# Performance work log

Measured on AMD Instinct MI355X. Metric: run time of the kernel, lower is better.

## Reference

```python
import jax, jax.numpy as jnp
import numpy as np

B, S, D, H = 8, 2048, 1024, 128  # batch, seq (== CONTEXT_WINDOW), embed dim, headspace


def setup_inputs() -> dict:
    key = jax.random.key(0)
    ks = jax.random.split(key, 7)
    scale = 1.0 / np.sqrt(D)
    return {
        "x": jax.random.normal(ks[0], (B, S, D), dtype=jnp.float32),
        "Wq": jax.random.normal(ks[1], (D, H), dtype=jnp.float32) * scale,
        "bq": jax.random.normal(ks[2], (H,), dtype=jnp.float32) * 0.01,
        "Wk": jax.random.normal(ks[3], (D, H), dtype=jnp.float32) * scale,
        "bk": jax.random.normal(ks[4], (H,), dtype=jnp.float32) * 0.01,
        "Wv": jax.random.normal(ks[5], (D, H), dtype=jnp.float32) * scale,
        "bv": jax.random.normal(ks[6], (H,), dtype=jnp.float32) * 0.01,
    }


def reference(x, Wq, bq, Wk, bk, Wv, bv):
    # x: [B, S, D]
    embedlen = x.shape[-1]
    q = x @ Wq + bq  # [B, S, H]
    k = x @ Wk + bk  # [B, S, H]
    v = x @ Wv + bv  # [B, S, H]
    # NOTE: original code MULTIPLIES by sqrt(embedlen) (embedlen = full embed dim) --
    # faithful reproduction of the source, not the standard 1/sqrt(head_dim).
    scale = jnp.sqrt(jnp.asarray(embedlen, dtype=x.dtype))
    scores = jnp.einsum("bsh,bth->bst", q, k) * scale  # [B, S, S]
    seqlen = x.shape[1]
    causal = jnp.tril(jnp.ones((seqlen, seqlen), dtype=bool))
    scores = jnp.where(causal, scores, -jnp.inf)
    attn = jax.nn.softmax(scores, axis=-1)
    return jnp.einsum("bst,bth->bsh", attn, v)  # [B, S, H]
```

## Files before the change

kernel.cpp:

```cpp
#include <hip/hip_runtime.h>
#include <math.h>

#define SEQ 2048
#define DIM 1024
#define HD  128
#define NB  8
#define M_TOT (NB * SEQ)

typedef __attribute__((ext_vector_type(8))) short   short8;
typedef __attribute__((ext_vector_type(4))) short   short4v;
typedef __attribute__((ext_vector_type(4))) float   floatx4;

__device__ __forceinline__ unsigned short f2bf(float f) {
    unsigned u = __builtin_bit_cast(unsigned, f);
    u += 0x7FFFu + ((u >> 16) & 1u);
    return (unsigned short)(u >> 16);
}
__device__ __forceinline__ float bf2f(unsigned short h) {
    unsigned u = ((unsigned)h) << 16;
    return __builtin_bit_cast(float, u);
}
__device__ __forceinline__ void async16(const void* g, void* l) {
    __builtin_amdgcn_global_load_lds(
        (const __attribute__((address_space(1))) unsigned int*)g,
        (__attribute__((address_space(3))) unsigned int*)l, 16, 0, 0);
}

#define MFMA16(a, b, c) __builtin_amdgcn_mfma_f32_16x16x32_bf16((a), (b), (c), 0, 0, 0)

__global__ __launch_bounds__(256) void wt_prep(
    const float* __restrict__ Wq, const float* __restrict__ Wk, const float* __restrict__ Wv,
    unsigned short* __restrict__ Wth, unsigned short* __restrict__ Wtl)
{
    int idx = blockIdx.x * 256 + threadIdx.x;
    int k   = idx & 1023;
    int n   = (idx >> 10) & 127;
    int mat = idx >> 17;
    const float* W = (mat == 0) ? Wq : (mat == 1) ? Wk : Wv;
    float v = W[k * HD + n];
    unsigned short hi = f2bf(v);
    Wth[idx] = hi;
    Wtl[idx] = f2bf(v - bf2f(hi));
}

__global__ __launch_bounds__(512, 4) void qkv_fused(
    const float* __restrict__ x,
    const unsigned short* __restrict__ Wth, const unsigned short* __restrict__ Wtl,
    const float* __restrict__ bq, const float* __restrict__ bk, const float* __restrict__ bv,
    unsigned short* __restrict__ Qh, unsigned short* __restrict__ Ql,
    unsigned short* __restrict__ Kh, unsigned short* __restrict__ Kl,
    unsigned short* __restrict__ Vt)
{
    __shared__ short lds[56 * 512];

    const int t    = threadIdx.x;
    const int lane = t & 63;
    const int w    = t >> 6;
    const int lrow = lane & 15;
    const int quad = lane >> 4;

    const int R0 = blockIdx.x * 64;
    const int z  = blockIdx.y;
    const int mh = w & 1;
    const int nh = w >> 1;

    auto stageB = [&](int k0, int qb) {
        #pragma unroll
        for (int i = 0; i < 3; ++i) {
            int f = i * 8 + w;
            if (f < 20) {
                int p   = (f >= 12);
                int ff  = p ? (f - 12) : f;
                int mat = ff >> 2, nfl = ff & 3;
                const unsigned short* src = (p ? Wtl : Wth) + (size_t)mat * (HD * DIM)
                    + (size_t)((z * 4 + nfl) * 16 + lrow) * DIM + k0 + quad * 8;
                async16(src, &lds[(qb * 28 + 8 + f) * 512 + lane * 8]);
            }
        }
    };

    const int arow = t >> 3;
    const int akk  = (t & 7) * 4;
    auto xload = [&](int k0) -> float4 {
        return *(const float4*)&x[(size_t)(R0 + arow) * DIM + k0 + akk];
    };
    auto stageA = [&](float4 xv, int qb) {
        float xf[4] = {xv.x, xv.y, xv.z, xv.w};
        short4v hv, lv;
        #pragma unroll
        for (int j = 0; j < 4; ++j) {
            unsigned short h = f2bf(xf[j]);
            hv[j] = (short)h;
            lv[j] = (short)f2bf(xf[j] - bf2f(h));
        }
        int mi = arow >> 4, lr = arow & 15, qd = akk >> 3, el = akk & 7;
        int base = (qb * 28 + mi * 2) * 512 + (qd * 16 + lr) * 8 + el;
        *(short4v*)&lds[base]       = hv;
        *(short4v*)&lds[base + 512] = lv;
    };

    floatx4 acc[2][3];
    const floatx4 zf = {0.f, 0.f, 0.f, 0.f};
    #pragma unroll
    for (int mi2 = 0; mi2 < 2; ++mi2)
        #pragma unroll
        for (int c = 0; c < 3; ++c) acc[mi2][c] = zf;

    auto compute = [&](int qb) {
        short8 a[2][2];
        #pragma unroll
        for (int mi2 = 0; mi2 < 2; ++mi2)
            #pragma unroll
            for (int p = 0; p < 2; ++p)
                a[mi2][p] = *(short8*)&lds[(qb * 28 + (mh * 2 + mi2) * 2 + p) * 512 + lane * 8];

        short8 bhq = *(short8*)&lds[(qb * 28 + 8 +  0 + nh) * 512 + lane * 8];
        short8 bhk = *(short8*)&lds[(qb * 28 + 8 +  4 + nh) * 512 + lane * 8];
        short8 bhv = *(short8*)&lds[(qb * 28 + 8 +  8 + nh) * 512 + lane * 8];
        short8 blq = *(short8*)&lds[(qb * 28 + 20 + 0 + nh) * 512 + lane * 8];
        short8 blk = *(short8*)&lds[(qb * 28 + 20 + 4 + nh) * 512 + lane * 8];

        #pragma unroll
        for (int mi2 = 0; mi2 < 2; ++mi2) {
            acc[mi2][0] = MFMA16(a[mi2][0], bhq, acc[mi2][0]);
            acc[mi2][1] = MFMA16(a[mi2][0], bhk, acc[mi2][1]);
            acc[mi2][2] = MFMA16(a[mi2][0], bhv, acc[mi2][2]);
            acc[mi2][0] = MFMA16(a[mi2][1], bhq, acc[mi2][0]);
            acc[mi2][1] = MFMA16(a[mi2][1], bhk, acc[mi2][1]);
            acc[mi2][0] = MFMA16(a[mi2][0], blq, acc[mi2][0]);
            acc[mi2][1] = MFMA16(a[mi2][0], blk, acc[mi2][1]);
        }
    };

    stageB(0, 0);
    stageA(xload(0), 0);
    float4 xn0 = xload(32);
    float4 xn1 = xload(64);

    for (int it = 0; it < 32; ++it) {
        __syncthreads();
        const int k0 = it * 32;
        const int q  = it & 1;

        if (it < 31) {
            stageB(k0 + 32, q ^ 1);
            stageA(xn0, q ^ 1);
            xn0 = xn1;
            int kx = (k0 + 96 <= DIM - 32) ? (k0 + 96) : (DIM - 32);
            xn1 = xload(kx);
        }

        compute(q);
    }

    const int col = (z * 4 + nh) * 16 + lrow;
    const float bqv = bq[col], bkv = bk[col], bvv = bv[col];
    #pragma unroll
    for (int mi2 = 0; mi2 < 2; ++mi2) {
        #pragma unroll
        for (int reg = 0; reg < 4; ++reg) {
            int gm = R0 + (mh * 2 + mi2) * 16 + quad * 4 + reg;
            float vq = (acc[mi2][0][reg] + bqv) * 32.0f;
            unsigned short h = f2bf(vq);
            Qh[(size_t)gm * HD + col] = h;
            Ql[(size_t)gm * HD + col] = f2bf(vq - bf2f(h));
            float vk = acc[mi2][1][reg] + bkv;
            h = f2bf(vk);
            Kh[(size_t)gm * HD + col] = h;
            Kl[(size_t)gm * HD + col] = f2bf(vk - bf2f(h));
            float vv = acc[mi2][2][reg] + bvv;
            int b = gm >> 11, s = gm & 2047;
            Vt[((size_t)b * HD + col) * SEQ + s] = f2bf(vv);
        }
    }
}

__global__ __launch_bounds__(256) void flash_attn(
    const unsigned short* __restrict__ Qh, const unsigned short* __restrict__ Ql,
    const unsigned short* __restrict__ Kh, const unsigned short* __restrict__ Kl,
    const unsigned short* __restrict__ Vt, float* __restrict__ out,
    float* __restrict__ Opart, float* __restrict__ ML, int split)
{
    __shared__ short lds[52 * 512];

    const int t    = threadIdx.x;
    const int lane = t & 63;
    const int w    = t >> 6;
    const int lrow = lane & 15;
    const int quad = lane >> 4;

    const int idx = blockIdx.x;
    const int b   = idx & 7;
    const int h   = split ? ((idx >> 3) & 1) : 0;
    const int s   = split ? (63 - (idx >> 4)) : (63 - (idx >> 3));
    const int T   = (s + 2) >> 1;
    const int Th  = (T + 1) >> 1;
    const int t0  = split ? (h ? Th : 0) : 0;
    const int t1  = split ? (h ? T : Th) : T;

    if (split && t0 >= t1) {
        float* op = Opart + (size_t)idx * 4096;
        for (int i = t; i < 4096; i += 256) op[i] = 0.0f;
        if (t < 32) { ML[(idx * 32 + t) * 2] = -1e30f; ML[(idx * 32 + t) * 2 + 1] = 0.0f; }
        return;
    }

    const int mh = w & 1;
    const int kh = w >> 1;
    const int R  = s * 32 + mh * 16;

    const size_t kbase = (size_t)b * SEQ * HD;
    const size_t vbase = (size_t)b * HD * SEQ;

    short8 qf[4][2];
    #pragma unroll
    for (int kc = 0; kc < 4; ++kc) {
        size_t off = kbase + (size_t)(R + lrow) * HD + kc * 32 + quad * 8;
        qf[kc][0] = *(const short8*)(Qh + off);
        qf[kc][1] = *(const short8*)(Ql + off);
    }

    const floatx4 zf = {0.f, 0.f, 0.f, 0.f};
    floatx4 accO[8];
    #pragma unroll
    for (int i = 0; i < 8; ++i) accO[i] = zf;
    float m_[4] = {-1e30f, -1e30f, -1e30f, -1e30f};
    float l_[4] = {0.f, 0.f, 0.f, 0.f};

    for (int it = t0; it < t1; ++it) {
        const int j0 = it * 64;
        __syncthreads();
        #pragma unroll
        for (int i = 0; i < 12; ++i) {
            int id = w * 12 + i;
            const unsigned short* src;
            if (id < 32) {
                int nt = id >> 3, kc = (id >> 1) & 3, p = id & 1;
                src = (p ? Kl : Kh) + kbase
                    + (size_t)(j0 + nt * 16 + lrow) * HD + kc * 32 + quad * 8;
            } else {
                int v = id - 32, df = v >> 1, kc = v & 1;
                src = Vt + vbase + (size_t)(df * 16 + lrow) * SEQ
                    + j0 + kc * 32 + quad * 8;
            }
            async16(src, &lds[id * 512 + lane * 8]);
        }
        __syncthreads();

        floatx4 S[2] = {zf, zf};
        #pragma unroll
        for (int ntl = 0; ntl < 2; ++ntl) {
            int nt = kh * 2 + ntl;
            #pragma unroll
            for (int kc = 0; kc < 4; ++kc) {
                short8 khf = *(short8*)&lds[(nt * 8 + kc * 2 + 0) * 512 + lane * 8];
                short8 klf = *(short8*)&lds[(nt * 8 + kc * 2 + 1) * 512 + lane * 8];
                S[ntl] = MFMA16(qf[kc][0], khf, S[ntl]);
                S[ntl] = MFMA16(qf[kc][0], klf, S[ntl]);
                S[ntl] = MFMA16(qf[kc][1], khf, S[ntl]);
            }
        }
        if (j0 + kh * 32 + 31 > R) {
            #pragma unroll
            for (int ntl = 0; ntl < 2; ++ntl) {
                int key = j0 + (kh * 2 + ntl) * 16 + lrow;
                #pragma unroll
                for (int reg = 0; reg < 4; ++reg) {
                    if (key > R + quad * 4 + reg) S[ntl][reg] = -INFINITY;
                }
            }
        }
        float alpha[4];
        #pragma unroll
        for (int reg = 0; reg < 4; ++reg) {
            float mx = fmaxf(S[0][reg], S[1][reg]);
            #pragma unroll
            for (int hh = 1; hh < 16; hh <<= 1) mx = fmaxf(mx, __shfl_xor(mx, hh));
            float mnew = fmaxf(fmaxf(m_[reg], mx), -1e30f);
            alpha[reg] = __expf(m_[reg] - mnew);
            m_[reg] = mnew;
            float p0 = __expf(S[0][reg] - mnew);
            float p1 = __expf(S[1][reg] - mnew);
            S[0][reg] = p0; S[1][reg] = p1;
            float ls = p0 + p1;
            #pragma unroll
            for (int hh = 1; hh < 16; hh <<= 1) ls += __shfl_xor(ls, hh);
            l_[reg] = l_[reg] * alpha[reg] + ls;
        }
        #pragma unroll
        for (int i = 0; i < 8; ++i)
            #pragma unroll
            for (int reg = 0; reg < 4; ++reg) accO[i][reg] *= alpha[reg];

        #pragma unroll
        for (int ntl = 0; ntl < 2; ++ntl) {
            #pragma unroll
            for (int reg = 0; reg < 4; ++reg) {
                int kloc = ntl * 16 + lrow;
                int jj = kloc & 7, q2 = (kloc >> 3) & 3;
                int lane2 = (quad * 4 + reg) + (q2 << 4);
                lds[(48 + w) * 512 + lane2 * 8 + jj] = (short)f2bf(S[ntl][reg]);
            }
        }
        short8 pf = *(short8*)&lds[(48 + w) * 512 + lane * 8];
        #pragma unroll
        for (int df = 0; df < 8; ++df) {
            short8 vf = *(short8*)&lds[(32 + df * 2 + kh) * 512 + lane * 8];
            accO[df] = MFMA16(pf, vf, accO[df]);
        }
    }

    __syncthreads();
    float* fl   = (float*)lds;
    float* Obuf = fl;
    float* mlb  = fl + 4096;
    if (lrow == 0) {
        #pragma unroll
        for (int reg = 0; reg < 4; ++reg) {
            int row = quad * 4 + reg;
            mlb[((kh * 2 + mh) * 16 + row) * 2 + 0] = m_[reg];
            mlb[((kh * 2 + mh) * 16 + row) * 2 + 1] = l_[reg];
        }
    }
    __syncthreads();
    float myw[4], Mrow[4], Drow[4];
    #pragma unroll
    for (int reg = 0; reg < 4; ++reg) {
        int row = quad * 4 + reg;
        float mo  = mlb[(((1 - kh) * 2 + mh) * 16 + row) * 2 + 0];
        float lo_ = mlb[(((1 - kh) * 2 + mh) * 16 + row) * 2 + 1];
        float M = fmaxf(m_[reg], mo);
        float d = l_[reg] * __expf(m_[reg] - M) + lo_ * __expf(mo - M);
        Mrow[reg] = M; Drow[reg] = d;
        myw[reg] = split ? __expf(m_[reg] - M) : (__expf(m_[reg] - M) / d);
    }
    if (kh == 0) {
        #pragma unroll
        for (int df = 0; df < 8; ++df)
            #pragma unroll
            for (int reg = 0; reg < 4; ++reg)
                Obuf[(mh * 16 + quad * 4 + reg) * 128 + df * 16 + lrow] =
                    accO[df][reg] * myw[reg];
    }
    __syncthreads();
    if (kh == 1) {
        if (split) {
            float* op = Opart + (size_t)idx * 4096;
            #pragma unroll
            for (int df = 0; df < 8; ++df) {
                #pragma unroll
                for (int reg = 0; reg < 4; ++reg) {
                    int row = mh * 16 + quad * 4 + reg;
                    op[row * 128 + df * 16 + lrow] =
                        Obuf[row * 128 + df * 16 + lrow] + accO[df][reg] * myw[reg];
                }
            }
            if (lrow == 0) {
                #pragma unroll
                for (int reg = 0; reg < 4; ++reg) {
                    int row = mh * 16 + quad * 4 + reg;
                    ML[(idx * 32 + row) * 2 + 0] = Mrow[reg];
                    ML[(idx * 32 + row) * 2 + 1] = Drow[reg];
                }
            }
        } else {
            #pragma unroll
            for (int df = 0; df < 8; ++df) {
                #pragma unroll
                for (int reg = 0; reg < 4; ++reg) {
                    float v = Obuf[(mh * 16 + quad * 4 + reg) * 128 + df * 16 + lrow]
                            + accO[df][reg] * myw[reg];
                    size_t o = ((size_t)(b * SEQ + R + quad * 4 + reg)) * HD + df * 16 + lrow;
                    out[o] = v;
                }
            }
        }
    }
}

__global__ __launch_bounds__(256) void splitk_merge(
    const float* __restrict__ Opart, const float* __restrict__ ML,
    float* __restrict__ out)
{
    int tid = blockIdx.x * 256 + threadIdx.x;
    int row = tid >> 5, c4 = tid & 31;
    int b = row >> 11, r = row & 2047, s = r >> 5, rr = r & 31;
    int i0 = ((63 - s) << 4) + b;
    int i1 = i0 + 8;
    float m0 = ML[(i0 * 32 + rr) * 2], l0 = ML[(i0 * 32 + rr) * 2 + 1];
    float m1 = ML[(i1 * 32 + rr) * 2], l1 = ML[(i1 * 32 + rr) * 2 + 1];
    float M  = fmaxf(m0, m1);
    float w0 = __expf(m0 - M), w1 = __expf(m1 - M);
    float inv = 1.0f / (w0 * l0 + w1 * l1);
    float4 a  = *(const float4*)&Opart[((size_t)i0 * 32 + rr) * 128 + c4 * 4];
    float4 bb = *(const float4*)&Opart[((size_t)i1 * 32 + rr) * 128 + c4 * 4];
    float4 o;
    o.x = (w0 * a.x + w1 * bb.x) * inv;
    o.y = (w0 * a.y + w1 * bb.y) * inv;
    o.z = (w0 * a.z + w1 * bb.z) * inv;
    o.w = (w0 * a.w + w1 * bb.w) * inv;
    *(float4*)&out[(size_t)row * 128 + c4 * 4] = o;
}

extern "C" void kernel_launch(void* const* d_in, const int* in_sizes, int n_in,
                              void* d_out, int out_size, void* d_ws, size_t ws_size,
                              hipStream_t stream) {
    const float* x  = (const float*)d_in[0];
    const float* Wq = (const float*)d_in[1];
    const float* bq = (const float*)d_in[2];
    const float* Wk = (const float*)d_in[3];
    const float* bk = (const float*)d_in[4];
    const float* Wv = (const float*)d_in[5];
    const float* bv = (const float*)d_in[6];
    float* out = (float*)d_out;

    unsigned short* Qh  = (unsigned short*)d_ws;
    unsigned short* Ql  = Qh  + (size_t)M_TOT * HD;
    unsigned short* Kh  = Ql  + (size_t)M_TOT * HD;
    unsigned short* Kl  = Kh  + (size_t)M_TOT * HD;
    unsigned short* Vt  = Kl  + (size_t)M_TOT * HD;
    unsigned short* Wth = Vt  + (size_t)M_TOT * HD;
    unsigned short* Wtl = Wth + (size_t)3 * HD * DIM;
    float* Opart = (float*)(Wtl + (size_t)3 * HD * DIM);
    float* ML    = Opart + (size_t)1024 * 32 * 128;

    const size_t need = 22544384ULL + 16777216ULL + 262144ULL;
    const int split = (ws_size >= need) ? 1 : 0;

    wt_prep<<<(3 * HD * DIM) / 256, 256, 0, stream>>>(Wq, Wk, Wv, Wth, Wtl);
    qkv_fused<<<dim3(256, 2), 512, 0, stream>>>(x, Wth, Wtl, bq, bk, bv, Qh, Ql, Kh, Kl, Vt);
    flash_attn<<<split ? 1024 : 512, 256, 0, stream>>>(Qh, Ql, Kh, Kl, Vt, out, Opart, ML, split);
    if (split) splitk_merge<<<2048, 256, 0, stream>>>(Opart, ML, out);
}
```

Baseline: 218.5 us.

## Load V fragments directly from global into registers instead of staging in LDS

V tiles are no longer staged into shared memory with async copies. Each wave now loads its V MFMA fragments straight from global into registers, half before the barrier and half after the softmax. LDS shrinks from 52 to 36 slots and launch bounds request 4 blocks per CU, aiming for higher occupancy and less LDS traffic. The cost is per-wave redundant global V loads (each kh-half is read by two waves), extra register pressure, and exposed global latency on the second half of the V loads.

Result: slower. 262.1 us (+20.0%).

```diff
diff --git a/kernel.cpp b/kernel.cpp
--- a/kernel.cpp
+++ b/kernel.cpp
@@ -175,13 +175,13 @@
     }
 }
 
-__global__ __launch_bounds__(256) void flash_attn(
+__global__ __launch_bounds__(256, 4) void flash_attn(
     const unsigned short* __restrict__ Qh, const unsigned short* __restrict__ Ql,
     const unsigned short* __restrict__ Kh, const unsigned short* __restrict__ Kl,
     const unsigned short* __restrict__ Vt, float* __restrict__ out,
     float* __restrict__ Opart, float* __restrict__ ML, int split)
 {
-    __shared__ short lds[52 * 512];
+    __shared__ short lds[36 * 512];
 
     const int t    = threadIdx.x;
     const int lane = t & 63;
@@ -231,20 +231,18 @@
         const int j0 = it * 64;
         __syncthreads();
         #pragma unroll
-        for (int i = 0; i < 12; ++i) {
-            int id = w * 12 + i;
-            const unsigned short* src;
-            if (id < 32) {
-                int nt = id >> 3, kc = (id >> 1) & 3, p = id & 1;
-                src = (p ? Kl : Kh) + kbase
-                    + (size_t)(j0 + nt * 16 + lrow) * HD + kc * 32 + quad * 8;
-            } else {
-                int v = id - 32, df = v >> 1, kc = v & 1;
-                src = Vt + vbase + (size_t)(df * 16 + lrow) * SEQ
-                    + j0 + kc * 32 + quad * 8;
-            }
+        for (int i = 0; i < 8; ++i) {
+            int id = w * 8 + i;
+            int nt = id >> 3, kc = (id >> 1) & 3, p = id & 1;
+            const unsigned short* src = (p ? Kl : Kh) + kbase
+                + (size_t)(j0 + nt * 16 + lrow) * HD + kc * 32 + quad * 8;
             async16(src, &lds[id * 512 + lane * 8]);
         }
+        short8 vfA[4];
+        #pragma unroll
+        for (int df = 0; df < 4; ++df)
+            vfA[df] = *(const short8*)(Vt + vbase + (size_t)(df * 16 + lrow) * SEQ
+                                       + j0 + kh * 32 + quad * 8);
         __syncthreads();
 
         floatx4 S[2] = {zf, zf};
@@ -299,15 +297,21 @@
                 int kloc = ntl * 16 + lrow;
                 int jj = kloc & 7, q2 = (kloc >> 3) & 3;
                 int lane2 = (quad * 4 + reg) + (q2 << 4);
-                lds[(48 + w) * 512 + lane2 * 8 + jj] = (short)f2bf(S[ntl][reg]);
-            }
-        }
-        short8 pf = *(short8*)&lds[(48 + w) * 512 + lane * 8];
-        #pragma unroll
-        for (int df = 0; df < 8; ++df) {
-            short8 vf = *(short8*)&lds[(32 + df * 2 + kh) * 512 + lane * 8];
-            accO[df] = MFMA16(pf, vf, accO[df]);
-        }
+                lds[(32 + w) * 512 + lane2 * 8 + jj] = (short)f2bf(S[ntl][reg]);
+            }
+        }
+        short8 vfB[4];
+        #pragma unroll
+        for (int df = 0; df < 4; ++df)
+            vfB[df] = *(const short8*)(Vt + vbase + (size_t)((df + 4) * 16 + lrow) * SEQ
+                                       + j0 + kh * 32 + quad * 8);
+        short8 pf = *(short8*)&lds[(32 + w) * 512 + lane * 8];
+        #pragma unroll
+        for (int df = 0; df < 4; ++df)
+            accO[df] = MFMA16(pf, vfA[df], accO[df]);
+        #pragma unroll
+        for (int df = 0; df < 4; ++df)
+            accO[df + 4] = MFMA16(pf, vfB[df], accO[df + 4]);
     }
 
     __syncthreads();
```

## Prefetch next K/V tile into registers while computing current tile

Applied to the files above, without the earlier changes.

Replaces the per-iteration async global-to-LDS copy plus two barriers with a register-staged software pipeline. The next K/V tile is loaded into registers at the top of each iteration and written to LDS after the current tile's compute. Global load latency can then overlap with the MFMA work. It also adds launch_bounds(256,3) to cap register use at three blocks per CU, which risks spills given the 12 extra short8 registers per thread.

Result: slower. 224.9 us (+3.0%).

```diff
diff --git a/kernel.cpp b/kernel.cpp
--- a/kernel.cpp
+++ b/kernel.cpp
@@ -175,7 +175,7 @@
     }
 }
 
-__global__ __launch_bounds__(256) void flash_attn(
+__global__ __launch_bounds__(256, 3) void flash_attn(
     const unsigned short* __restrict__ Qh, const unsigned short* __restrict__ Ql,
     const unsigned short* __restrict__ Kh, const unsigned short* __restrict__ Kl,
     const unsigned short* __restrict__ Vt, float* __restrict__ out,
@@ -220,6 +220,33 @@
         qf[kc][1] = *(const short8*)(Ql + off);
     }
 
+    short8 Kn[8];
+    short8 Vn[4];
+    auto issueKV = [&](int it) {
+        const int j0 = it * 64;
+        #pragma unroll
+        for (int i = 0; i < 8; ++i) {
+            int id = w * 8 + i;
+            int nt = id >> 3, kc = (id >> 1) & 3, p = id & 1;
+            Kn[i] = *(const short8*)((p ? Kl : Kh) + kbase
+                    + (size_t)(j0 + nt * 16 + lrow) * HD + kc * 32 + quad * 8);
+        }
+        #pragma unroll
+        for (int i = 0; i < 4; ++i) {
+            int v = w * 4 + i, df = v >> 1, kc = v & 1;
+            Vn[i] = *(const short8*)(Vt + vbase + (size_t)(df * 16 + lrow) * SEQ
+                    + j0 + kc * 32 + quad * 8);
+        }
+    };
+    auto writeKV = [&]() {
+        #pragma unroll
+        for (int i = 0; i < 8; ++i)
+            *(short8*)&lds[(w * 8 + i) * 512 + lane * 8] = Kn[i];
+        #pragma unroll
+        for (int i = 0; i < 4; ++i)
+            *(short8*)&lds[(32 + w * 4 + i) * 512 + lane * 8] = Vn[i];
+    };
+
     const floatx4 zf = {0.f, 0.f, 0.f, 0.f};
     floatx4 accO[8];
     #pragma unroll
@@ -227,25 +254,13 @@
     float m_[4] = {-1e30f, -1e30f, -1e30f, -1e30f};
     float l_[4] = {0.f, 0.f, 0.f, 0.f};
 
+    issueKV(t0);
+    writeKV();
+    __syncthreads();
+
     for (int it = t0; it < t1; ++it) {
         const int j0 = it * 64;
-        __syncthreads();
-        #pragma unroll
-        for (int i = 0; i < 12; ++i) {
-            int id = w * 12 + i;
-            const unsigned short* src;
-            if (id < 32) {
-                int nt = id >> 3, kc = (id >> 1) & 3, p = id & 1;
-                src = (p ? Kl : Kh) + kbase
-                    + (size_t)(j0 + nt * 16 + lrow) * HD + kc * 32 + quad * 8;
-            } else {
-                int v = id - 32, df = v >> 1, kc = v & 1;
-                src = Vt + vbase + (size_t)(df * 16 + lrow) * SEQ
-                    + j0 + kc * 32 + quad * 8;
-            }
-            async16(src, &lds[id * 512 + lane * 8]);
-        }
-        __syncthreads();
+        if (it + 1 < t1) issueKV(it + 1);
 
         floatx4 S[2] = {zf, zf};
         #pragma unroll
@@ -307,6 +322,12 @@
         for (int df = 0; df < 8; ++df) {
             short8 vf = *(short8*)&lds[(32 + df * 2 + kh) * 512 + lane * 8];
             accO[df] = MFMA16(pf, vf, accO[df]);
+        }
+
+        __syncthreads();
+        if (it + 1 < t1) {
+            writeKV();
+            __syncthreads();
         }
     }
 
```

## Double-buffer K/V tiles in LDS with 32-key steps and prefetch

Applied to the files above, without the earlier changes.

Shrinks the key tile per iteration from 64 to 32 keys and double-buffers the K and V staging in LDS. The next tile's async global-to-LDS loads are issued before computing on the current one, which drops one barrier per iteration and is meant to hide load latency behind the MFMA work. Each wave now computes one 16-key score tile instead of two, and the P buffer is zero-initialised so the unused half reads as zero. In exchange the loop runs twice as many iterations, each with less MFMA work, so per-iteration softmax, shuffle and rescale overhead doubles.

Result: slower. 223.0 us (+2.0%).

```diff
diff --git a/kernel.cpp b/kernel.cpp
--- a/kernel.cpp
+++ b/kernel.cpp
@@ -193,7 +193,7 @@
     const int b   = idx & 7;
     const int h   = split ? ((idx >> 3) & 1) : 0;
     const int s   = split ? (63 - (idx >> 4)) : (63 - (idx >> 3));
-    const int T   = (s + 2) >> 1;
+    const int T   = s + 1;
     const int Th  = (T + 1) >> 1;
     const int t0  = split ? (h ? Th : 0) : 0;
     const int t1  = split ? (h ? T : Th) : T;
@@ -220,6 +220,24 @@
         qf[kc][1] = *(const short8*)(Ql + off);
     }
 
+    auto stage = [&](int it, int qb) {
+        const int j0 = it * 32;
+        #pragma unroll
+        for (int i = 0; i < 6; ++i) {
+            int id = w * 6 + i;
+            const unsigned short* src;
+            if (id < 16) {
+                int nt = id >> 3, kc = (id >> 1) & 3, p = id & 1;
+                src = (p ? Kl : Kh) + kbase
+                    + (size_t)(j0 + nt * 16 + lrow) * HD + kc * 32 + quad * 8;
+            } else {
+                int df = id - 16;
+                src = Vt + vbase + (size_t)(df * 16 + lrow) * SEQ + j0 + quad * 8;
+            }
+            async16(src, &lds[(qb * 24 + id) * 512 + lane * 8]);
+        }
+    };
+
     const floatx4 zf = {0.f, 0.f, 0.f, 0.f};
     floatx4 accO[8];
     #pragma unroll
@@ -227,62 +245,46 @@
     float m_[4] = {-1e30f, -1e30f, -1e30f, -1e30f};
     float l_[4] = {0.f, 0.f, 0.f, 0.f};
 
+    {
+        short8 z8 = {0, 0, 0, 0, 0, 0, 0, 0};
+        *(short8*)&lds[(48 + w) * 512 + lane * 8] = z8;
+    }
+
+    stage(t0, 0);
+
     for (int it = t0; it < t1; ++it) {
-        const int j0 = it * 64;
+        const int q = (it - t0) & 1;
         __syncthreads();
-        #pragma unroll
-        for (int i = 0; i < 12; ++i) {
-            int id = w * 12 + i;
-            const unsigned short* src;
-            if (id < 32) {
-                int nt = id >> 3, kc = (id >> 1) & 3, p = id & 1;
-                src = (p ? Kl : Kh) + kbase
-                    + (size_t)(j0 + nt * 16 + lrow) * HD + kc * 32 + quad * 8;
-            } else {
-                int v = id - 32, df = v >> 1, kc = v & 1;
-                src = Vt + vbase + (size_t)(df * 16 + lrow) * SEQ
-                    + j0 + kc * 32 + quad * 8;
-            }
-            async16(src, &lds[id * 512 + lane * 8]);
-        }
-        __syncthreads();
-
-        floatx4 S[2] = {zf, zf};
-        #pragma unroll
-        for (int ntl = 0; ntl < 2; ++ntl) {
-            int nt = kh * 2 + ntl;
-            #pragma unroll
-            for (int kc = 0; kc < 4; ++kc) {
-                short8 khf = *(short8*)&lds[(nt * 8 + kc * 2 + 0) * 512 + lane * 8];
-                short8 klf = *(short8*)&lds[(nt * 8 + kc * 2 + 1) * 512 + lane * 8];
-                S[ntl] = MFMA16(qf[kc][0], khf, S[ntl]);
-                S[ntl] = MFMA16(qf[kc][0], klf, S[ntl]);
-                S[ntl] = MFMA16(qf[kc][1], khf, S[ntl]);
-            }
-        }
-        if (j0 + kh * 32 + 31 > R) {
-            #pragma unroll
-            for (int ntl = 0; ntl < 2; ++ntl) {
-                int key = j0 + (kh * 2 + ntl) * 16 + lrow;
-                #pragma unroll
-                for (int reg = 0; reg < 4; ++reg) {
-                    if (key > R + quad * 4 + reg) S[ntl][reg] = -INFINITY;
-                }
-            }
+        if (it + 1 < t1) stage(it + 1, q ^ 1);
+        const int j0 = it * 32;
+
+        floatx4 S = zf;
+        #pragma unroll
+        for (int kc = 0; kc < 4; ++kc) {
+            short8 khf = *(short8*)&lds[(q * 24 + kh * 8 + kc * 2 + 0) * 512 + lane * 8];
+            short8 klf = *(short8*)&lds[(q * 24 + kh * 8 + kc * 2 + 1) * 512 + lane * 8];
+            S = MFMA16(qf[kc][0], khf, S);
+            S = MFMA16(qf[kc][0], klf, S);
+            S = MFMA16(qf[kc][1], khf, S);
+        }
+        if (j0 + kh * 16 + 15 > R) {
+            int key = j0 + kh * 16 + lrow;
+            #pragma unroll
+            for (int reg = 0; reg < 4; ++reg)
+                if (key > R + quad * 4 + reg) S[reg] = -INFINITY;
         }
         float alpha[4];
         #pragma unroll
         for (int reg = 0; reg < 4; ++reg) {
-            float mx = fmaxf(S[0][reg], S[1][reg]);
+            float mx = S[reg];
             #pragma unroll
             for (int hh = 1; hh < 16; hh <<= 1) mx = fmaxf(mx, __shfl_xor(mx, hh));
             float mnew = fmaxf(fmaxf(m_[reg], mx), -1e30f);
             alpha[reg] = __expf(m_[reg] - mnew);
             m_[reg] = mnew;
-            float p0 = __expf(S[0][reg] - mnew);
-            float p1 = __expf(S[1][reg] - mnew);
-            S[0][reg] = p0; S[1][reg] = p1;
-            float ls = p0 + p1;
+            float p0 = __expf(S[reg] - mnew);
+            S[reg] = p0;
+            float ls = p0;
             #pragma unroll
             for (int hh = 1; hh < 16; hh <<= 1) ls += __shfl_xor(ls, hh);
             l_[reg] = l_[reg] * alpha[reg] + ls;
@@ -293,19 +295,16 @@
             for (int reg = 0; reg < 4; ++reg) accO[i][reg] *= alpha[reg];
 
         #pragma unroll
-        for (int ntl = 0; ntl < 2; ++ntl) {
-            #pragma unroll
-            for (int reg = 0; reg < 4; ++reg) {
-                int kloc = ntl * 16 + lrow;
-                int jj = kloc & 7, q2 = (kloc >> 3) & 3;
-                int lane2 = (quad * 4 + reg) + (q2 << 4);
-                lds[(48 + w) * 512 + lane2 * 8 + jj] = (short)f2bf(S[ntl][reg]);
-            }
+        for (int reg = 0; reg < 4; ++reg) {
+            int kloc = kh * 16 + lrow;
+            int jj = kloc & 7, q2 = (kloc >> 3) & 3;
+            int lane2 = (quad * 4 + reg) + (q2 << 4);
+            lds[(48 + w) * 512 + lane2 * 8 + jj] = (short)f2bf(S[reg]);
         }
         short8 pf = *(short8*)&lds[(48 + w) * 512 + lane * 8];
         #pragma unroll
         for (int df = 0; df < 8; ++df) {
-            short8 vf = *(short8*)&lds[(32 + df * 2 + kh) * 512 + lane * 8];
+            short8 vf = *(short8*)&lds[(q * 24 + 16 + df) * 512 + lane * 8];
             accO[df] = MFMA16(pf, vf, accO[df]);
         }
     }
```
